# Kernel tuning notes

Hardware: AMD Instinct MI355X
Metric: run time of the kernel (lower is better)

Reference implementation:

```python
import jax, jax.numpy as jnp
import numpy as np

D_MODEL = 1024
N_HEADS = 16
D_HEAD = D_MODEL // N_HEADS


def setup_inputs() -> dict:
    key = jax.random.key(0)
    k1, k2, k3 = jax.random.split(key, 3)
    B, T = 2, 2048
    x = jax.random.normal(k1, (B, T, D_MODEL), dtype=jnp.float32)
    # Linear weights stored as (in, out), equivalent to torch W^T
    w_qkv = jax.random.normal(k2, (D_MODEL, 3 * D_MODEL), dtype=jnp.float32) * (D_MODEL ** -0.5)
    w_proj = jax.random.normal(k3, (D_MODEL, D_MODEL), dtype=jnp.float32) * (D_MODEL ** -0.5)
    return {"x": x, "w_qkv": w_qkv, "w_proj": w_proj}


def reference(x, w_qkv, w_proj):
    B, T, C = x.shape
    qkv = x @ w_qkv                                   # (B, T, 3C)
    qkv = qkv.reshape(B, T, 3, N_HEADS, D_HEAD)
    q, k, v = qkv[:, :, 0], qkv[:, :, 1], qkv[:, :, 2]  # (B, T, H, dh)
    q = q.transpose(0, 2, 1, 3)                        # (B, H, T, dh)
    k = k.transpose(0, 2, 1, 3)
    v = v.transpose(0, 2, 1, 3)
    scale = 1.0 / jnp.sqrt(jnp.float32(D_HEAD))
    scores = jnp.einsum('bhqd,bhkd->bhqk', q, k) * scale  # (B, H, T, T)
    causal = jnp.tril(jnp.ones((T, T), dtype=bool))
    scores = jnp.where(causal, scores, jnp.float32(-jnp.inf))
    w = jax.nn.softmax(scores, axis=-1)
    ctx = jnp.einsum('bhqk,bhkd->bhqd', w, v)          # (B, H, T, dh)
    ctx = ctx.transpose(0, 2, 1, 3).reshape(B, T, C)
    return ctx @ w_proj
```

## Files before the change

kernel.cpp:

```cpp
#include <hip/hip_runtime.h>
#include <hip/hip_bf16.h>
#include <math.h>
#include <stdint.h>

#define D_MODEL 1024
#define NHEADS  16
#define DHEAD   64
#define BATCH   2
#define SEQ     2048
#define ROWS    (BATCH*SEQ)

#define NEG_BIG (-1e30f)
#define QSCALE  0.18033688011112042f

typedef __bf16 bf16v8 __attribute__((ext_vector_type(8)));
typedef short  shortv8 __attribute__((ext_vector_type(8)));
typedef short  shortv4 __attribute__((ext_vector_type(4)));
typedef float  floatv4 __attribute__((ext_vector_type(4)));
typedef unsigned short ush;

__device__ __forceinline__ ush f2b(float f) {
  return __builtin_bit_cast(ush, (__bf16)f);
}

__device__ __forceinline__ void async16(ush* lds, const ush* g) {
  __builtin_amdgcn_global_load_lds(
      (const __attribute__((address_space(1))) void*)g,
      (__attribute__((address_space(3))) void*)lds, 16, 0, 0);
}

__global__ __launch_bounds__(256)
void prep(const uint32_t* __restrict__ x, ush* __restrict__ xb,
          const void* __restrict__ wqkv, ush* __restrict__ wqkvT,
          const void* __restrict__ wproj, ush* __restrict__ wprojT,
          int* __restrict__ flagp) {
  __shared__ int sflag;
  __shared__ __align__(16) ush tile[64][72];

  int bid = blockIdx.x;
  int t   = threadIdx.x;

  if (t < 64) {
    uint32_t e = (x[t] >> 7) & 0xFF;
    unsigned long long m = __ballot(e >= 96 && e <= 144);
    if (t == 0) sflag = (__popcll(m) >= 32) ? 1 : 0;
  }
  __syncthreads();
  int isbf = sflag;
  if (bid == 0 && t == 0) *flagp = isbf;

  if (bid < 2048) {
    size_t i = (size_t)bid * 256 + t;
    if (isbf) {
      ((shortv8*)xb)[i] = ((const shortv8*)x)[i];
    } else {
      const floatv4* p = ((const floatv4*)x) + i * 2;
      floatv4 a = p[0], b = p[1];
      shortv8 o;
#pragma unroll
      for (int j = 0; j < 4; ++j) { o[j] = (short)f2b(a[j]); o[4+j] = (short)f2b(b[j]); }
      ((shortv8*)xb)[i] = o;
    }
  } else {
    const void* W; ush* Wt; int N, b2;
    const int K = 1024;
    if (bid < 2816) { W = wqkv;  Wt = wqkvT;  N = 3072; b2 = bid - 2048; }
    else            { W = wproj; Wt = wprojT; N = 1024; b2 = bid - 2816; }
    int tiles_n = N >> 6;
    int tk = b2 / tiles_n;
    int tn = b2 % tiles_n;
    int r  = t >> 2;
    int c8 = (t & 3) * 8;

    if (isbf) {
      const ush* src = (const ush*)W + (size_t)(tk*64 + r) * N + tn*64;
#pragma unroll
      for (int c = 0; c < 2; ++c)
        *(shortv8*)&tile[r][c8 + c*32] = *(const shortv8*)&src[c8 + c*32];
    } else {
      const float* src = (const float*)W + (size_t)(tk*64 + r) * N + tn*64;
#pragma unroll
      for (int c = 0; c < 2; ++c) {
        const floatv4* p = (const floatv4*)&src[c8 + c*32];
        floatv4 a = p[0], b = p[1];
        shortv8 o;
#pragma unroll
        for (int j = 0; j < 4; ++j) { o[j] = (short)f2b(a[j]); o[4+j] = (short)f2b(b[j]); }
        *(shortv8*)&tile[r][c8 + c*32] = o;
      }
    }
    __syncthreads();
    ush* dst = Wt + (size_t)(tn*64 + r) * K + tk*64;
#pragma unroll
    for (int c = 0; c < 2; ++c) {
      int k8 = c8 + c*32;
      shortv8 v;
#pragma unroll
      for (int j = 0; j < 8; ++j) v[j] = (short)tile[k8 + j][r];
      *(shortv8*)&dst[k8] = v;
    }
  }
}

#define MFMA16(a,b,c) __builtin_amdgcn_mfma_f32_16x16x32_bf16(a,b,c,0,0,0)

__global__ __launch_bounds__(512, 2)
void gemm_qkv(const ush* __restrict__ A, const ush* __restrict__ Bt,
              ush* __restrict__ qb_, ush* __restrict__ kb_, ush* __restrict__ vb_) {
  __shared__ __align__(16) ush smem[65536];
  const int K = 1024;
  const int tiles_n = 12;
  int raw = blockIdx.x;
  int bid = (raw & 7) * 24 + (raw >> 3);
  int m0 = (bid / tiles_n) * 256;
  int n0 = (bid % tiles_n) * 256;
  int t    = threadIdx.x;
  int lane = t & 63;
  int w    = t >> 6;
  int wr   = w >> 2;
  int wc   = w & 3;
  int lr   = lane & 15;
  int quad = lane >> 4;
  int r8   = lane >> 3;
  int s8   = lane & 7;
  int g8   = s8 ^ r8;

  int aeo = 2*w + (w>>2)*8;
  int alo = aeo + 8;
  int beo = (w>>1)*8 + (w&1)*2;
  int blo = beo + 4;

  const ush* gAe0 = A  + (size_t)(m0 + aeo*8     + r8)*K + g8*8;
  const ush* gAe1 = gAe0 + (size_t)8*K;
  const ush* gAl0 = A  + (size_t)(m0 + alo*8     + r8)*K + g8*8;
  const ush* gAl1 = gAl0 + (size_t)8*K;
  const ush* gBe0 = Bt + (size_t)(n0 + beo*8     + r8)*K + g8*8;
  const ush* gBe1 = gBe0 + (size_t)8*K;
  const ush* gBl0 = Bt + (size_t)(n0 + blo*8     + r8)*K + g8*8;
  const ush* gBl1 = gBl0 + (size_t)8*K;

  int lAe0 = aeo*512,         lAe1 = lAe0 + 512;
  int lAl0 = alo*512,         lAl1 = lAl0 + 512;
  int lBe0 = 32768 + beo*512, lBe1 = lBe0 + 512;
  int lBl0 = 32768 + blo*512, lBl1 = lBl0 + 512;

  floatv4 acc[4][8] = {};
  bf16v8 af[4][2];
  bf16v8 bf[4][2];

  int sk0 = ((quad    ) ^ (lr & 7)) * 8;
  int sk1 = ((quad + 4) ^ (lr & 7)) * 8;

  async16(&smem[lAe0], gAe0); async16(&smem[lAe1], gAe1);
  async16(&smem[lBe0], gBe0); async16(&smem[lBe1], gBe1);
  async16(&smem[lBl0], gBl0); async16(&smem[lBl1], gBl1);
  async16(&smem[lAl0], gAl0); async16(&smem[lAl1], gAl1);

  for (int kt = 0; kt < 16; ++kt) {
    int cur = kt & 1, nx = cur ^ 1;
    int kn  = (kt + 1 < 16) ? (kt + 1) : 15;
    int ko  = kn * 64;
    int nb  = nx * 16384;

    const ush* Ab = &smem[cur*16384 + (wr*128 + lr)*64];
    const ush* Bb = &smem[32768 + cur*16384 + (wc*64 + lr)*64];

    asm volatile("s_waitcnt vmcnt(4)" ::: "memory");
    __builtin_amdgcn_s_barrier();

#pragma unroll
    for (int mi = 0; mi < 4; ++mi) {
      af[mi][0] = *(const bf16v8*)&Ab[mi*1024 + sk0];
      af[mi][1] = *(const bf16v8*)&Ab[mi*1024 + sk1];
    }
#pragma unroll
    for (int ni = 0; ni < 2; ++ni) {
      bf[ni][0] = *(const bf16v8*)&Bb[ni*1024 + sk0];
      bf[ni][1] = *(const bf16v8*)&Bb[ni*1024 + sk1];
    }
    async16(&smem[nb + lAe0], gAe0 + ko); async16(&smem[nb + lAe1], gAe1 + ko);
    __builtin_amdgcn_s_setprio(1);
#pragma unroll
    for (int ni = 0; ni < 2; ++ni)
#pragma unroll
      for (int mi = 0; mi < 4; ++mi)
#pragma unroll
        for (int ks = 0; ks < 2; ++ks)
          acc[ni][mi] = MFMA16(bf[ni][ks], af[mi][ks], acc[ni][mi]);
    __builtin_amdgcn_s_setprio(0);

    asm volatile("s_waitcnt vmcnt(4)" ::: "memory");
    __builtin_amdgcn_s_barrier();

#pragma unroll
    for (int ni = 0; ni < 2; ++ni) {
      bf[2+ni][0] = *(const bf16v8*)&Bb[(2+ni)*1024 + sk0];
      bf[2+ni][1] = *(const bf16v8*)&Bb[(2+ni)*1024 + sk1];
    }
    async16(&smem[nb + lBe0], gBe0 + ko); async16(&smem[nb + lBe1], gBe1 + ko);
    __builtin_amdgcn_s_setprio(1);
#pragma unroll
    for (int ni = 0; ni < 2; ++ni)
#pragma unroll
      for (int mi = 0; mi < 4; ++mi)
#pragma unroll
        for (int ks = 0; ks < 2; ++ks)
          acc[2+ni][mi] = MFMA16(bf[2+ni][ks], af[mi][ks], acc[2+ni][mi]);
    __builtin_amdgcn_s_setprio(0);

    asm volatile("s_waitcnt vmcnt(4)" ::: "memory");
    __builtin_amdgcn_s_barrier();

#pragma unroll
    for (int mi = 0; mi < 4; ++mi) {
      af[mi][0] = *(const bf16v8*)&Ab[4096 + mi*1024 + sk0];
      af[mi][1] = *(const bf16v8*)&Ab[4096 + mi*1024 + sk1];
    }
    async16(&smem[nb + lBl0], gBl0 + ko); async16(&smem[nb + lBl1], gBl1 + ko);
    __builtin_amdgcn_s_setprio(1);
#pragma unroll
    for (int ni = 0; ni < 2; ++ni)
#pragma unroll
      for (int mi = 0; mi < 4; ++mi)
#pragma unroll
        for (int ks = 0; ks < 2; ++ks)
          acc[ni][4+mi] = MFMA16(bf[ni][ks], af[mi][ks], acc[ni][4+mi]);
    __builtin_amdgcn_s_setprio(0);

    __builtin_amdgcn_s_barrier();

    async16(&smem[nb + lAl0], gAl0 + ko); async16(&smem[nb + lAl1], gAl1 + ko);
    __builtin_amdgcn_s_setprio(1);
#pragma unroll
    for (int ni = 0; ni < 2; ++ni)
#pragma unroll
      for (int mi = 0; mi < 4; ++mi)
#pragma unroll
        for (int ks = 0; ks < 2; ++ks)
          acc[2+ni][4+mi] = MFMA16(bf[2+ni][ks], af[mi][ks], acc[2+ni][4+mi]);
    __builtin_amdgcn_s_setprio(0);
  }

  asm volatile("s_waitcnt vmcnt(0)" ::: "memory");
  __builtin_amdgcn_s_barrier();

  int s   = n0 >> 10;
  int h   = ((n0 & 1023) + wc*64) >> 6;
  int b   = (m0 + wr*128) >> 11;
  int bh  = b*16 + h;
  int ttw = (m0 + wr*128) & 2047;

  if (s < 2) {
    ush* dst = (s == 0) ? qb_ : kb_;
    float sc = (s == 0) ? QSCALE : 1.0f;
#pragma unroll
    for (int ni = 0; ni < 4; ++ni) {
      int d4 = ni*16 + quad*4;
#pragma unroll
      for (int mi = 0; mi < 8; ++mi) {
        int tt = ttw + mi*16 + lr;
        shortv4 v4;
#pragma unroll
        for (int r = 0; r < 4; ++r) v4[r] = (short)f2b(acc[ni][mi][r] * sc);
        *(shortv4*)&dst[((size_t)bh*SEQ + tt)*64 + d4] = v4;
      }
    }
  } else {
    ush* L = &smem[w*4096];
#pragma unroll
    for (int th = 0; th < 2; ++th) {
      int tw = ttw + th*64;
#pragma unroll
      for (int ni = 0; ni < 4; ++ni) {
#pragma unroll
        for (int r = 0; r < 4; ++r) {
          int dl = ni*16 + quad*4 + r;
          shortv4 p4;
#pragma unroll
          for (int j = 0; j < 4; ++j) p4[j] = (short)f2b(acc[ni][th*4 + j][r]);
          int slot = (lr >> 1) ^ (dl & 7);
          *(shortv4*)&L[dl*64 + slot*8 + (lr & 1)*4] = p4;
        }
      }
#pragma unroll
      for (int p = 0; p < 8; ++p) {
        int dl = p*8 + (lane >> 3);
        int c8 = lane & 7;
        int slot = c8 ^ (dl & 7);
        shortv8 v = *(shortv8*)&L[dl*64 + slot*8];
        *(shortv8*)&vb_[((size_t)bh*64 + dl)*SEQ + tw + c8*8] = v;
      }
    }
  }
}

__global__ __launch_bounds__(256, 4)
void gemm_bt(const ush* __restrict__ A, const ush* __restrict__ Bt,
             void* __restrict__ Cp, const int* __restrict__ flag,
             int ldc, int tiles_n) {
  __shared__ __align__(16) ush smem[12288];
  const int K = 1024;
  int raw = blockIdx.x;
  int bid = ((raw & 7) << 6) | (raw >> 3);
  int m0 = (bid / tiles_n) * 64;
  int n0 = (bid % tiles_n) * 128;
  int t    = threadIdx.x;
  int lane = t & 63;
  int w    = t >> 6;
  int wm   = (w >> 1) * 32;
  int wn   = (w & 1) * 64;
  int lr   = lane & 15;
  int quad = lane >> 4;
  floatv4 acc[4][2] = {};
  int r16 = lane >> 2;
  int g4  = (lane & 3) ^ (r16 & 3);
  const ush* gA0 = A  + (size_t)(m0 + 16*w + r16)*K + g4*8;
  const ush* gB0 = Bt + (size_t)(n0 + 32*w + r16)*K + g4*8;
  const ush* gB1 = gB0 + (size_t)16*K;
  int fs = (quad ^ (lr & 3)) * 8;

  async16(&smem[(16*w)*32], gA0);
  async16(&smem[4096 + (32*w)*32], gB0);
  async16(&smem[4096 + (32*w+16)*32], gB1);

  for (int kk = 0; kk < K; kk += 32) {
    int cur = (kk >> 5) & 1;
    __syncthreads();
    if (kk + 32 < K) {
      int nx = cur ^ 1;
      async16(&smem[nx*2048 + (16*w)*32], gA0 + kk + 32);
      async16(&smem[4096 + nx*4096 + (32*w)*32], gB0 + kk + 32);
      async16(&smem[4096 + nx*4096 + (32*w+16)*32], gB1 + kk + 32);
    }
    bf16v8 af[2], bfr[4];
#pragma unroll
    for (int j = 0; j < 2; ++j)
      af[j] = *(bf16v8*)&smem[cur*2048 + (wm + j*16 + lr)*32 + fs];
#pragma unroll
    for (int i = 0; i < 4; ++i)
      bfr[i] = *(bf16v8*)&smem[4096 + cur*4096 + (wn + i*16 + lr)*32 + fs];
#pragma unroll
    for (int i = 0; i < 4; ++i)
#pragma unroll
      for (int j = 0; j < 2; ++j)
        acc[i][j] = __builtin_amdgcn_mfma_f32_16x16x32_bf16(bfr[i], af[j],
                                                            acc[i][j], 0, 0, 0);
  }

  int f32out = (flag != nullptr) && (*flag == 0);
  if (f32out) {
    float* Cf = (float*)Cp;
#pragma unroll
    for (int i = 0; i < 4; ++i) {
      int nb = n0 + wn + i*16 + quad*4;
#pragma unroll
      for (int j = 0; j < 2; ++j) {
        int row = m0 + wm + j*16 + lr;
        *(floatv4*)&Cf[(size_t)row*ldc + nb] = acc[i][j];
      }
    }
  } else {
    __hip_bfloat16* Cb = (__hip_bfloat16*)Cp;
#pragma unroll
    for (int i = 0; i < 4; ++i) {
      int nb = n0 + wn + i*16 + quad*4;
#pragma unroll
      for (int j = 0; j < 2; ++j) {
        int row = m0 + wm + j*16 + lr;
        shortv4 v4;
#pragma unroll
        for (int r = 0; r < 4; ++r) v4[r] = (short)f2b(acc[i][j][r]);
        *(shortv4*)&((ush*)Cb)[(size_t)row*ldc + nb] = v4;
      }
    }
  }
}

#define PSTR 72

__device__ __forceinline__ void softpack(const floatv4* s, int qw, int kb0,
                                         bool diag, ush* PsW, int quad, int lr) {
  if (diag) {
#pragma unroll
    for (int r = 0; r < 4; ++r) {
      int qv = qw + quad*4 + r;
      shortv4 p4;
#pragma unroll
      for (int j = 0; j < 4; ++j) {
        float z = (kb0 + 16*j + lr > qv) ? NEG_BIG : s[j][r];
        p4[j] = (short)f2b(__builtin_amdgcn_exp2f(z));
      }
      *(shortv4*)&PsW[(quad*4 + r)*PSTR + lr*4] = p4;
    }
  } else {
#pragma unroll
    for (int r = 0; r < 4; ++r) {
      shortv4 p4;
#pragma unroll
      for (int j = 0; j < 4; ++j)
        p4[j] = (short)f2b(__builtin_amdgcn_exp2f(s[j][r]));
      *(shortv4*)&PsW[(quad*4 + r)*PSTR + lr*4] = p4;
    }
  }
}

__global__ __launch_bounds__(512, 4)
void attn_fwd(const ush* __restrict__ qb_, const ush* __restrict__ kb_,
              const ush* __restrict__ vb_, __hip_bfloat16* __restrict__ ctx) {
  __shared__ __align__(16) ush Ks[2][64*64];
  __shared__ __align__(16) ush Vt[2][64*64];
  __shared__ __align__(16) ush Ps[8][16*PSTR];

  int raw = blockIdx.x;
  int bid = ((raw & 7) << 6) | (raw >> 3);
  int g   = (bid & 15) ^ (((bid >> 5) & 1) ? 15 : 0);
  int bh  = bid >> 4;
  int h   = bh & 15;
  int b   = bh >> 4;

  int t = threadIdx.x, w8 = t >> 6, lane = t & 63, lr = lane & 15, quad = lane >> 4;

  const ush* qh = qb_ + (size_t)bh * SEQ * 64;
  const ush* kh = kb_ + (size_t)bh * SEQ * 64;
  const ush* vh = vb_ + (size_t)bh * 64 * SEQ;

  int qw     = g*128 + w8*16;
  int myLast = 2*g + (w8 >> 2);
  int wj     = w8 & 3;

  const ush* qp = qh + (size_t)(qw + lr)*64;
  bf16v8 qf0 = *(const bf16v8*)&qp[quad*8];
  bf16v8 qf1 = *(const bf16v8*)&qp[32 + quad*8];

  floatv4 acc[4] = {}, acl = {};

  bf16v8 ones;
#pragma unroll
  for (int j = 0; j < 8; ++j) ones[j] = (__bf16)1.0f;

  int r8 = lane >> 3;
  int s8 = lane & 7;
  int g8 = s8 ^ r8;
  const ush* kg = kh + (size_t)(8*w8 + r8)*64 + g8*8;
  const ush* vg = vh + (size_t)(8*w8 + r8)*SEQ + g8*8;
  int lo = (8*w8)*64;

  int sl0 = quad ^ (lr & 7);
  int sl1 = (quad + 4) ^ (lr & 7);

  int ntiles = 2*g + 2;

  async16(&Ks[0][lo], kg);
  async16(&Vt[0][lo], vg);

  for (int tk = 0; tk < ntiles; ++tk) {
    int cur = tk & 1;
    __syncthreads();
    if (tk + 1 < ntiles) {
      int nx = cur ^ 1;
      async16(&Ks[nx][lo], kg + (size_t)(tk + 1) * 64 * 64);
      async16(&Vt[nx][lo], vg + (size_t)(tk + 1) * 64);
    }

    bool live = (tk <= myLast);
    if (live) {
      int kb0 = tk * 64;
      bool diag = (tk == myLast);

      floatv4 s[4] = {};
      __builtin_amdgcn_s_setprio(1);
#pragma unroll
      for (int j = 0; j < 4; ++j) {
        if (!diag || j <= wj) {
          int row = 16*j + lr;
          bf16v8 kf0 = *(bf16v8*)&Ks[cur][row*64 + sl0*8];
          bf16v8 kf1 = *(bf16v8*)&Ks[cur][row*64 + sl1*8];
          s[j] = MFMA16(qf0, kf0, s[j]);
          s[j] = MFMA16(qf1, kf1, s[j]);
        }
      }
      __builtin_amdgcn_s_setprio(0);

      softpack(s, qw, kb0, diag, &Ps[w8][0], quad, lr);

      bf16v8 pf0 = *(bf16v8*)&Ps[w8][lr*PSTR + quad*8];
      bf16v8 pf1 = *(bf16v8*)&Ps[w8][lr*PSTR + 32 + quad*8];

      __builtin_amdgcn_s_setprio(1);
      acl = MFMA16(pf0, ones, acl);
      acl = MFMA16(pf1, ones, acl);

#pragma unroll
      for (int c = 0; c < 4; ++c) {
        int row = 16*c + lr;
        bf16v8 vf0 = *(bf16v8*)&Vt[cur][row*64 + sl0*8];
        bf16v8 vf1 = *(bf16v8*)&Vt[cur][row*64 + sl1*8];
        acc[c] = MFMA16(pf0, vf0, acc[c]);
        acc[c] = MFMA16(pf1, vf1, acc[c]);
      }
      __builtin_amdgcn_s_setprio(0);
    }
  }

#pragma unroll
  for (int r = 0; r < 4; ++r) {
    float inv = 1.0f / fmaxf(acl[r], 1e-30f);
    size_t o = (size_t)(b*SEQ + qw + quad*4 + r) * D_MODEL + h*64;
#pragma unroll
    for (int c = 0; c < 4; ++c)
      ctx[o + c*16 + lr] = __float2bfloat16(acc[c][r] * inv);
  }
}

extern "C" void kernel_launch(void* const* d_in, const int* in_sizes, int n_in,
                              void* d_out, int out_size, void* d_ws, size_t ws_size,
                              hipStream_t stream) {
  const void* x      = d_in[0];
  const void* w_qkv  = d_in[1];
  const void* w_proj = d_in[2];

  int* flag   = (int*)d_ws;
  ush* xb     = (ush*)d_ws + 8;
  ush* wqkvT  = xb     + (size_t)ROWS * D_MODEL;
  ush* wprojT = wqkvT  + (size_t)3072 * 1024;
  ush* qbuf   = wprojT + (size_t)1024 * 1024;
  ush* kbuf   = qbuf   + (size_t)32 * SEQ * 64;
  ush* vbuf   = kbuf   + (size_t)32 * SEQ * 64;
  ush* ctx    = xb;

  prep<<<3072, 256, 0, stream>>>((const uint32_t*)x, xb,
                                 w_qkv, wqkvT, w_proj, wprojT, flag);

  gemm_qkv<<<192, 512, 0, stream>>>(xb, wqkvT, qbuf, kbuf, vbuf);

  attn_fwd<<<BATCH * NHEADS * 16, 512, 0, stream>>>(
      qbuf, kbuf, vbuf, (__hip_bfloat16*)ctx);

  gemm_bt<<<(ROWS/64)*(1024/128), 256, 0, stream>>>(
      ctx, wprojT, d_out, flag, 1024, 1024/128);
}
```

Baseline: 175.7 us.

## Split long causal query tiles across two blocks with a combine kernel

Attention work for the eight longest query tiles per head is split along the key dimension into two blocks, raising the grid from 512 to 768 blocks for better load balance across CUs. The halves write unnormalized fp32 partial accumulators and row sums, and a new combine kernel adds them and normalizes into ctx. This works without rescaling because softmax uses a fixed offset rather than a running max. Launch bounds also go from 4 to 6 blocks per CU. The cost is an extra kernel launch, fp32 partial-buffer traffic, and possible register pressure from the tighter occupancy target.

```diff
diff --git a/kernel.cpp b/kernel.cpp
--- a/kernel.cpp
+++ b/kernel.cpp
@@ -404,19 +404,31 @@
   }
 }
 
-__global__ __launch_bounds__(512, 4)
+__global__ __launch_bounds__(512, 6)
 void attn_fwd(const ush* __restrict__ qb_, const ush* __restrict__ kb_,
-              const ush* __restrict__ vb_, __hip_bfloat16* __restrict__ ctx) {
+              const ush* __restrict__ vb_, __hip_bfloat16* __restrict__ ctx,
+              float* __restrict__ pacc, float* __restrict__ pacl) {
   __shared__ __align__(16) ush Ks[2][64*64];
   __shared__ __align__(16) ush Vt[2][64*64];
   __shared__ __align__(16) ush Ps[8][16*PSTR];
 
   int raw = blockIdx.x;
-  int bid = ((raw & 7) << 6) | (raw >> 3);
-  int g   = (bid & 15) ^ (((bid >> 5) & 1) ? 15 : 0);
-  int bh  = bid >> 4;
+  int bid = (raw & 7) * 96 + (raw >> 3);
+  int bh  = bid / 24;
+  int pid = bid % 24;
   int h   = bh & 15;
   int b   = bh >> 4;
+
+  int g, t0, t1, half; bool split;
+  if (pid < 16) {
+    int j = pid >> 1;
+    g = 8 + j; half = pid & 1; split = true;
+    t0 = half ? (g + 1) : 0;
+    t1 = half ? (2*g + 2) : (g + 1);
+  } else {
+    g = 23 - pid; half = 0; split = false;
+    t0 = 0; t1 = 2*g + 2;
+  }
 
   int t = threadIdx.x, w8 = t >> 6, lane = t & 63, lr = lane & 15, quad = lane >> 4;
 
@@ -448,17 +460,15 @@
   int sl0 = quad ^ (lr & 7);
   int sl1 = (quad + 4) ^ (lr & 7);
 
-  int ntiles = 2*g + 2;
-
-  async16(&Ks[0][lo], kg);
-  async16(&Vt[0][lo], vg);
-
-  for (int tk = 0; tk < ntiles; ++tk) {
-    int cur = tk & 1;
+  async16(&Ks[0][lo], kg + (size_t)t0 * 4096);
+  async16(&Vt[0][lo], vg + (size_t)t0 * 64);
+
+  for (int tk = t0; tk < t1; ++tk) {
+    int cur = (tk - t0) & 1;
     __syncthreads();
-    if (tk + 1 < ntiles) {
+    if (tk + 1 < t1) {
       int nx = cur ^ 1;
-      async16(&Ks[nx][lo], kg + (size_t)(tk + 1) * 64 * 64);
+      async16(&Ks[nx][lo], kg + (size_t)(tk + 1) * 4096);
       async16(&Vt[nx][lo], vg + (size_t)(tk + 1) * 64);
     }
 
@@ -502,13 +512,58 @@
     }
   }
 
-#pragma unroll
-  for (int r = 0; r < 4; ++r) {
-    float inv = 1.0f / fmaxf(acl[r], 1e-30f);
-    size_t o = (size_t)(b*SEQ + qw + quad*4 + r) * D_MODEL + h*64;
-#pragma unroll
-    for (int c = 0; c < 4; ++c)
-      ctx[o + c*16 + lr] = __float2bfloat16(acc[c][r] * inv);
+  if (!split) {
+#pragma unroll
+    for (int r = 0; r < 4; ++r) {
+      float inv = 1.0f / fmaxf(acl[r], 1e-30f);
+      size_t o = (size_t)(b*SEQ + qw + quad*4 + r) * D_MODEL + h*64;
+#pragma unroll
+      for (int c = 0; c < 4; ++c)
+        ctx[o + c*16 + lr] = __float2bfloat16(acc[c][r] * inv);
+    }
+  } else {
+    int slot = (bh*8 + (g - 8))*2 + half;
+    float* pa = pacc + (size_t)slot * 8192;
+#pragma unroll
+    for (int r = 0; r < 4; ++r) {
+      int row = w8*16 + quad*4 + r;
+#pragma unroll
+      for (int c = 0; c < 4; ++c)
+        pa[row*64 + c*16 + lr] = acc[c][r];
+    }
+    if (lr == 0) {
+#pragma unroll
+      for (int r = 0; r < 4; ++r)
+        pacl[(size_t)slot*128 + w8*16 + quad*4 + r] = acl[r];
+    }
+  }
+}
+
+__global__ __launch_bounds__(256)
+void attn_combine(const float* __restrict__ pacc, const float* __restrict__ pacl,
+                  __hip_bfloat16* __restrict__ ctx) {
+  int blk = blockIdx.x;
+  int bh  = blk >> 3, j = blk & 7;
+  int g   = 8 + j;
+  int h   = bh & 15, b = bh >> 4;
+  int t   = threadIdx.x;
+  int row = t >> 1;
+  int c0  = (t & 1) * 32;
+
+  const float* a0 = pacc + (size_t)blk * 2 * 8192 + row*64;
+  const float* a1 = a0 + 8192;
+  float l = pacl[(size_t)blk*2*128 + row] + pacl[(size_t)blk*2*128 + 128 + row];
+  float inv = 1.0f / fmaxf(l, 1e-30f);
+  size_t o = (size_t)(b*SEQ + g*128 + row) * D_MODEL + h*64 + c0;
+
+#pragma unroll
+  for (int cc = 0; cc < 32; cc += 4) {
+    floatv4 x0 = *(const floatv4*)&a0[c0 + cc];
+    floatv4 x1 = *(const floatv4*)&a1[c0 + cc];
+    shortv4 v4;
+#pragma unroll
+    for (int r = 0; r < 4; ++r) v4[r] = (short)f2b((x0[r] + x1[r]) * inv);
+    *(shortv4*)&((ush*)ctx)[o + cc] = v4;
   }
 }
 
@@ -526,6 +581,8 @@
   ush* qbuf   = wprojT + (size_t)1024 * 1024;
   ush* kbuf   = qbuf   + (size_t)32 * SEQ * 64;
   ush* vbuf   = kbuf   + (size_t)32 * SEQ * 64;
+  float* pacc = (float*)(vbuf + (size_t)32 * SEQ * 64);
+  float* pacl = pacc + (size_t)512 * 8192;
   ush* ctx    = xb;
 
   prep<<<3072, 256, 0, stream>>>((const uint32_t*)x, xb,
@@ -533,8 +590,10 @@
 
   gemm_qkv<<<192, 512, 0, stream>>>(xb, wqkvT, qbuf, kbuf, vbuf);
 
-  attn_fwd<<<BATCH * NHEADS * 16, 512, 0, stream>>>(
-      qbuf, kbuf, vbuf, (__hip_bfloat16*)ctx);
+  attn_fwd<<<768, 512, 0, stream>>>(
+      qbuf, kbuf, vbuf, (__hip_bfloat16*)ctx, pacc, pacl);
+
+  attn_combine<<<256, 256, 0, stream>>>(pacc, pacl, (__hip_bfloat16*)ctx);
 
   gemm_bt<<<(ROWS/64)*(1024/128), 256, 0, stream>>>(
       ctx, wprojT, d_out, flag, 1024, 1024/128);
```

Measured after the change: 172.0 us. 1.02x faster.
